# Kernel optimization log

Hardware: AMD Instinct MI355X
Metric: run time of the kernel (lower is better)

The kernel has to match this reference:

```python
import jax, jax.numpy as jnp
import numpy as np

D_MODEL = 256
NHEAD = 8
DHEAD = D_MODEL // NHEAD
LN_EPS = 1e-5
ATTN_EPS = 1e-6


def layer_norm(x, gamma, beta):
    mu = jnp.mean(x, axis=-1, keepdims=True)
    var = jnp.mean(jnp.square(x - mu), axis=-1, keepdims=True)
    return (x - mu) * jax.lax.rsqrt(var + LN_EPS) * gamma + beta


def setup_inputs() -> dict:
    key = jax.random.key(0)
    ks = jax.random.split(key, 12)
    B, L, S = 8, 4096, 4096
    s = 1.0 / np.sqrt(D_MODEL)
    return {
        "x": jax.random.normal(ks[0], (B, L, D_MODEL), jnp.float32),
        "source": jax.random.normal(ks[1], (B, S, D_MODEL), jnp.float32),
        "wq": jax.random.normal(ks[2], (D_MODEL, D_MODEL), jnp.float32) * s,
        "wk": jax.random.normal(ks[3], (D_MODEL, D_MODEL), jnp.float32) * s,
        "wv": jax.random.normal(ks[4], (D_MODEL, D_MODEL), jnp.float32) * s,
        "wmerge": jax.random.normal(ks[5], (D_MODEL, D_MODEL), jnp.float32) * s,
        "w1": jax.random.normal(ks[6], (2 * D_MODEL, D_MODEL), jnp.float32) * s,
        "w2": jax.random.normal(ks[7], (D_MODEL, 2 * D_MODEL), jnp.float32) * (1.0 / np.sqrt(2 * D_MODEL)),
        "g1": jnp.ones((D_MODEL,), jnp.float32),
        "b1": jnp.zeros((D_MODEL,), jnp.float32),
        "g2": jnp.ones((D_MODEL,), jnp.float32),
        "b2": jnp.zeros((D_MODEL,), jnp.float32),
    }


def reference(x, source, wq, wk, wv, wmerge, w1, w2, g1, b1, g2, b2):
    B, L, _ = x.shape
    S = source.shape[1]
    # QKV projections (bias-free Linear: y = x @ W^T), split into heads
    q = (x @ wq.T).reshape(B, L, NHEAD, DHEAD)
    k = (source @ wk.T).reshape(B, S, NHEAD, DHEAD)
    v = (source @ wv.T).reshape(B, S, NHEAD, DHEAD)
    # LinearAttention (LoFTR): feature map elu(.)+1, kernelized attention
    Q = jax.nn.elu(q) + 1.0
    K = jax.nn.elu(k) + 1.0
    v_len = jnp.asarray(S, v.dtype)
    values = v / v_len
    KV = jnp.einsum('bshd,bshv->bhdv', K, values)        # [B,H,D,D]
    Z = 1.0 / (jnp.einsum('blhd,bhd->blh', Q, K.sum(axis=1)) + ATTN_EPS)
    attended = jnp.einsum('blhd,bhdv,blh->blhv', Q, KV, Z) * v_len
    # merge + residual LN
    message = attended.reshape(B, L, D_MODEL) @ wmerge.T
    x = x + layer_norm(message, g1, b1)
    # MLP (d -> 2d -> d, ReLU) + residual LN
    h = jax.nn.relu(x @ w1.T) @ w2.T
    x = x + layer_norm(h, g2, b2)
    return x
```

## Files before the change

kernel.cpp:

```cpp
#include <hip/hip_runtime.h>

#define DM 256
#define SEQ 4096

typedef __attribute__((ext_vector_type(8))) short bf16x8;
typedef __attribute__((ext_vector_type(4))) float f32x4;

#define MFMA16(a, b, c) __builtin_amdgcn_mfma_f32_16x16x32_bf16(a, b, c, 0, 0, 0)

__device__ __forceinline__ short f2bf(float f) {
    union { float f; unsigned u; } c; c.f = f;
    unsigned r = (c.u + 0x7FFFu + ((c.u >> 16) & 1u)) >> 16;
    return (short)r;
}
__device__ __forceinline__ float bf2f(short s) {
    union { unsigned u; float f; } c; c.u = ((unsigned)(unsigned short)s) << 16; return c.f;
}
__device__ __forceinline__ bf16x8 pack8(float4 a, float4 b) {
    bf16x8 r;
    r[0] = f2bf(a.x); r[1] = f2bf(a.y); r[2] = f2bf(a.z); r[3] = f2bf(a.w);
    r[4] = f2bf(b.x); r[5] = f2bf(b.y); r[6] = f2bf(b.z); r[7] = f2bf(b.w);
    return r;
}

__global__ __launch_bounds__(256) void kWconv(const float* __restrict__ wq, const float* __restrict__ wk,
                                              const float* __restrict__ wv, const float* __restrict__ wm,
                                              const float* __restrict__ w1, const float* __restrict__ w2,
                                              short* __restrict__ dstws) {
    int blk = blockIdx.x;
    const float* src; short* dst;
    if (blk < 32)       { src = wq; dst = dstws;          }
    else if (blk < 64)  { src = wk; dst = dstws + 65536;  blk -= 32; }
    else if (blk < 96)  { src = wv; dst = dstws + 131072; blk -= 64; }
    else if (blk < 128) { src = wm; dst = dstws + 196608; blk -= 96; }
    else if (blk < 192) { src = w1; dst = dstws + 262144; blk -= 128; }
    else                { src = w2; dst = dstws + 393216; blk -= 192; }
    int idx = (blk * 256 + threadIdx.x) * 8;
    float4 f0 = *(const float4*)(src + idx), f1 = *(const float4*)(src + idx + 4);
    *(bf16x8*)(dst + idx) = pack8(f0, f1);
}

__global__ __launch_bounds__(256) void kA(const float* __restrict__ src,
                                          const short* __restrict__ wk, const short* __restrict__ wv,
                                          float* __restrict__ kv_part, float* __restrict__ ksum_part) {
    __shared__ char lds[65536];
    int t = threadIdx.x, lane = t & 63, w = t >> 6, r16 = lane & 15, g = lane >> 4;
    int b = blockIdx.x >> 6, blk = blockIdx.x & 63;
    const float* S = src + ((size_t)b * SEQ + blk * 64) * DM;
    char* kT = lds + w * 16384;
    char* vT = kT + 8192;
    f32x4 zz = {0.f, 0.f, 0.f, 0.f};
    f32x4 ak[4][4], av[4][4];
#pragma unroll
    for (int mi = 0; mi < 4; mi++)
#pragma unroll
        for (int ni = 0; ni < 4; ni++) { ak[mi][ni] = zz; av[mi][ni] = zz; }
#pragma unroll
    for (int kt = 0; kt < 8; kt++) {
        bf16x8 A[4], Bk[4], Bv[4];
#pragma unroll
        for (int mi = 0; mi < 4; mi++) {
            const float* p = S + (mi * 16 + r16) * DM + kt * 32 + g * 8;
            float4 f0 = *(const float4*)p, f1 = *(const float4*)(p + 4);
            A[mi] = pack8(f0, f1);
        }
#pragma unroll
        for (int ni = 0; ni < 4; ni++) {
            int n = w * 64 + ni * 16 + r16;
            Bk[ni] = *(const bf16x8*)(wk + n * DM + kt * 32 + g * 8);
            Bv[ni] = *(const bf16x8*)(wv + n * DM + kt * 32 + g * 8);
        }
#pragma unroll
        for (int mi = 0; mi < 4; mi++)
#pragma unroll
            for (int ni = 0; ni < 4; ni++) {
                ak[mi][ni] = MFMA16(A[mi], Bk[ni], ak[mi][ni]);
                av[mi][ni] = MFMA16(A[mi], Bv[ni], av[mi][ni]);
            }
    }
    float ksp[4] = {0.f, 0.f, 0.f, 0.f};
#pragma unroll
    for (int mi = 0; mi < 4; mi++)
#pragma unroll
        for (int ni = 0; ni < 4; ni++)
#pragma unroll
            for (int j = 0; j < 4; j++) {
                float q = ak[mi][ni][j];
                float e = q > 0.f ? q + 1.f : __expf(q);
                ksp[ni] += e;
                int srow = mi * 16 + g * 4 + j, feat = ni * 16 + r16;
                int by = (feat * 128 + srow * 2) ^ ((feat & 7) << 4);
                *(short*)(kT + by) = f2bf(e);
                *(short*)(vT + by) = f2bf(av[mi][ni][j]);
            }
    __syncthreads();
    f32x4 kv[2][2][2];
#pragma unroll
    for (int h = 0; h < 2; h++)
#pragma unroll
        for (int vi = 0; vi < 2; vi++)
#pragma unroll
            for (int di = 0; di < 2; di++) kv[h][vi][di] = zz;
#pragma unroll
    for (int h = 0; h < 2; h++)
#pragma unroll
        for (int st = 0; st < 2; st++) {
            bf16x8 Af[2], Bf[2];
#pragma unroll
            for (int vi = 0; vi < 2; vi++) {
                int row = h * 32 + vi * 16 + r16;
                Af[vi] = *(const bf16x8*)(vT + ((row * 128 + (st * 32 + g * 8) * 2) ^ ((row & 7) << 4)));
            }
#pragma unroll
            for (int di = 0; di < 2; di++) {
                int row = h * 32 + di * 16 + r16;
                Bf[di] = *(const bf16x8*)(kT + ((row * 128 + (st * 32 + g * 8) * 2) ^ ((row & 7) << 4)));
            }
#pragma unroll
            for (int vi = 0; vi < 2; vi++)
#pragma unroll
                for (int di = 0; di < 2; di++) kv[h][vi][di] = MFMA16(Af[vi], Bf[di], kv[h][vi][di]);
        }
    float* kvp = kv_part + ((size_t)(b * 64 + blk) * 8 + w * 2) * 1024;
#pragma unroll
    for (int h = 0; h < 2; h++)
#pragma unroll
        for (int vi = 0; vi < 2; vi++)
#pragma unroll
            for (int di = 0; di < 2; di++)
#pragma unroll
                for (int j = 0; j < 4; j++) {
                    int v = vi * 16 + g * 4 + j, d = di * 16 + r16;
                    kvp[h * 1024 + v * 32 + d] = kv[h][vi][di][j];
                }
#pragma unroll
    for (int ni = 0; ni < 4; ni++) {
        ksp[ni] += __shfl_xor(ksp[ni], 16);
        ksp[ni] += __shfl_xor(ksp[ni], 32);
    }
    if (lane < 16) {
        float* kp = ksum_part + (size_t)(b * 64 + blk) * 256 + w * 64;
#pragma unroll
        for (int ni = 0; ni < 4; ni++) kp[ni * 16 + lane] = ksp[ni];
    }
}

__global__ __launch_bounds__(256) void kA2(const float* __restrict__ kv_part, const float* __restrict__ ksum_part,
                                           short* __restrict__ kvt_bf, float* __restrict__ ksum) {
    int bh = blockIdx.x, b = bh >> 3, h = bh & 7, t = threadIdx.x;
#pragma unroll
    for (int i = 0; i < 4; i++) {
        int e = t + i * 256;
        float s = 0.f;
        for (int blk = 0; blk < 64; blk++)
            s += kv_part[((size_t)(b * 64 + blk) * 8 + h) * 1024 + e];
        kvt_bf[(size_t)bh * 1024 + e] = f2bf(s);
    }
    if (t < 32) {
        float s = 0.f;
        for (int blk = 0; blk < 64; blk++)
            s += ksum_part[(size_t)(b * 64 + blk) * 256 + h * 32 + t];
        ksum[bh * 32 + t] = s;
    }
}

__global__ __launch_bounds__(256) void kB(const float* __restrict__ x,
                                          const short* __restrict__ wq_bf, const short* __restrict__ wm_bf,
                                          const short* __restrict__ kvt_bf, const float* __restrict__ ksum,
                                          const float* __restrict__ g1, const float* __restrict__ b1,
                                          short* __restrict__ x1_ws) {
    __shared__ char xt[32768];
    __shared__ char qa[32768];
    __shared__ float ksum_l[256];
    __shared__ float red[64][4][2];
    int t = threadIdx.x, lane = t & 63, w = t >> 6, r16 = lane & 15, g = lane >> 4;
    int b = blockIdx.x >> 6, lb = blockIdx.x & 63, l0 = lb * 64;
    const float* xb = x + ((size_t)b * SEQ + l0) * DM;
    {
        int c8 = t & 31, r0 = t >> 5;
#pragma unroll
        for (int i = 0; i < 8; i++) {
            int row = r0 + i * 8;
            const float* p = xb + row * DM + c8 * 8;
            float4 f0 = *(const float4*)p, f1 = *(const float4*)(p + 4);
            int by = (row * 512 + c8 * 16) ^ ((row & 7) << 4);
            *(bf16x8*)(xt + by) = pack8(f0, f1);
        }
        ksum_l[t] = ksum[b * 256 + t];
    }
    __syncthreads();
    f32x4 zz = {0.f, 0.f, 0.f, 0.f};
    f32x4 acc[4][4];
#pragma unroll
    for (int mi = 0; mi < 4; mi++)
#pragma unroll
        for (int ni = 0; ni < 4; ni++) acc[mi][ni] = zz;
#pragma unroll
    for (int kt = 0; kt < 8; kt++) {
        bf16x8 A[4], Bf[4];
#pragma unroll
        for (int mi = 0; mi < 4; mi++) {
            int row = mi * 16 + r16;
            A[mi] = *(const bf16x8*)(xt + ((row * 512 + (kt * 32 + g * 8) * 2) ^ ((row & 7) << 4)));
        }
#pragma unroll
        for (int ni = 0; ni < 4; ni++)
            Bf[ni] = *(const bf16x8*)(wq_bf + (w * 64 + ni * 16 + r16) * DM + kt * 32 + g * 8);
#pragma unroll
        for (int mi = 0; mi < 4; mi++)
#pragma unroll
            for (int ni = 0; ni < 4; ni++) acc[mi][ni] = MFMA16(A[mi], Bf[ni], acc[mi][ni]);
    }
    float ks[2][2];
    ks[0][0] = ksum_l[(w * 2) * 32 + r16];     ks[0][1] = ksum_l[(w * 2) * 32 + 16 + r16];
    ks[1][0] = ksum_l[(w * 2 + 1) * 32 + r16]; ks[1][1] = ksum_l[(w * 2 + 1) * 32 + 16 + r16];
    float Zr[4][2][4];
#pragma unroll
    for (int mi = 0; mi < 4; mi++)
#pragma unroll
        for (int j = 0; j < 4; j++) {
#pragma unroll
            for (int ni = 0; ni < 4; ni++) {
                float q = acc[mi][ni][j];
                acc[mi][ni][j] = q > 0.f ? q + 1.f : __expf(q);
            }
            float d0 = acc[mi][0][j] * ks[0][0] + acc[mi][1][j] * ks[0][1];
            float d1 = acc[mi][2][j] * ks[1][0] + acc[mi][3][j] * ks[1][1];
#pragma unroll
            for (int m = 1; m < 16; m <<= 1) { d0 += __shfl_xor(d0, m); d1 += __shfl_xor(d1, m); }
            Zr[mi][0][j] = 1.f / (d0 + 1e-6f);
            Zr[mi][1][j] = 1.f / (d1 + 1e-6f);
        }
#pragma unroll
    for (int mi = 0; mi < 4; mi++)
#pragma unroll
        for (int ni = 0; ni < 4; ni++)
#pragma unroll
            for (int j = 0; j < 4; j++) {
                int row = mi * 16 + g * 4 + j, col = w * 64 + ni * 16 + r16;
                *(short*)(qa + ((row * 512 + col * 2) ^ ((row & 7) << 4))) = f2bf(acc[mi][ni][j]);
            }
    __syncthreads();
    f32x4 at[2][4][2];
#pragma unroll
    for (int h = 0; h < 2; h++)
#pragma unroll
        for (int mi = 0; mi < 4; mi++)
#pragma unroll
            for (int vi = 0; vi < 2; vi++) at[h][mi][vi] = zz;
#pragma unroll
    for (int h = 0; h < 2; h++) {
        int hh = w * 2 + h;
        bf16x8 A2[4], B2[2];
#pragma unroll
        for (int mi = 0; mi < 4; mi++) {
            int row = mi * 16 + r16, col = hh * 32 + g * 8;
            A2[mi] = *(const bf16x8*)(qa + ((row * 512 + col * 2) ^ ((row & 7) << 4)));
        }
        const short* kvb = kvt_bf + (size_t)(b * 8 + hh) * 1024;
#pragma unroll
        for (int vi = 0; vi < 2; vi++)
            B2[vi] = *(const bf16x8*)(kvb + (vi * 16 + r16) * 32 + g * 8);
#pragma unroll
        for (int mi = 0; mi < 4; mi++)
#pragma unroll
            for (int vi = 0; vi < 2; vi++) at[h][mi][vi] = MFMA16(A2[mi], B2[vi], at[h][mi][vi]);
    }
    __syncthreads();
#pragma unroll
    for (int h = 0; h < 2; h++)
#pragma unroll
        for (int mi = 0; mi < 4; mi++)
#pragma unroll
            for (int vi = 0; vi < 2; vi++)
#pragma unroll
                for (int j = 0; j < 4; j++) {
                    int row = mi * 16 + g * 4 + j, col = (w * 2 + h) * 32 + vi * 16 + r16;
                    float val = at[h][mi][vi][j] * Zr[mi][h][j];
                    *(short*)(qa + ((row * 512 + col * 2) ^ ((row & 7) << 4))) = f2bf(val);
                }
    __syncthreads();
    f32x4 am[4][4];
#pragma unroll
    for (int mi = 0; mi < 4; mi++)
#pragma unroll
        for (int ni = 0; ni < 4; ni++) am[mi][ni] = zz;
#pragma unroll
    for (int kt = 0; kt < 8; kt++) {
        bf16x8 A[4], Bf[4];
#pragma unroll
        for (int mi = 0; mi < 4; mi++) {
            int row = mi * 16 + r16;
            A[mi] = *(const bf16x8*)(qa + ((row * 512 + (kt * 32 + g * 8) * 2) ^ ((row & 7) << 4)));
        }
#pragma unroll
        for (int ni = 0; ni < 4; ni++)
            Bf[ni] = *(const bf16x8*)(wm_bf + (w * 64 + ni * 16 + r16) * DM + kt * 32 + g * 8);
#pragma unroll
        for (int mi = 0; mi < 4; mi++)
#pragma unroll
            for (int ni = 0; ni < 4; ni++) am[mi][ni] = MFMA16(A[mi], Bf[ni], am[mi][ni]);
    }
#pragma unroll
    for (int mi = 0; mi < 4; mi++)
#pragma unroll
        for (int j = 0; j < 4; j++) {
            float s = am[mi][0][j] + am[mi][1][j] + am[mi][2][j] + am[mi][3][j];
            float s2 = am[mi][0][j] * am[mi][0][j] + am[mi][1][j] * am[mi][1][j] +
                       am[mi][2][j] * am[mi][2][j] + am[mi][3][j] * am[mi][3][j];
#pragma unroll
            for (int m = 1; m < 16; m <<= 1) { s += __shfl_xor(s, m); s2 += __shfl_xor(s2, m); }
            if (r16 == 0) { int row = mi * 16 + g * 4 + j; red[row][w][0] = s; red[row][w][1] = s2; }
        }
    __syncthreads();
    float g1v[4], b1v[4];
#pragma unroll
    for (int ni = 0; ni < 4; ni++) { int col = w * 64 + ni * 16 + r16; g1v[ni] = g1[col]; b1v[ni] = b1[col]; }
#pragma unroll
    for (int mi = 0; mi < 4; mi++)
#pragma unroll
        for (int j = 0; j < 4; j++) {
            int row = mi * 16 + g * 4 + j;
            float mu = (red[row][0][0] + red[row][1][0] + red[row][2][0] + red[row][3][0]) * (1.f / DM);
            float ex2 = (red[row][0][1] + red[row][1][1] + red[row][2][1] + red[row][3][1]) * (1.f / DM);
            float rstd = rsqrtf(ex2 - mu * mu + 1e-5f);
#pragma unroll
            for (int ni = 0; ni < 4; ni++) {
                int col = w * 64 + ni * 16 + r16;
                float xv = bf2f(*(const short*)(xt + ((row * 512 + col * 2) ^ ((row & 7) << 4))));
                float x1v = xv + (am[mi][ni][j] - mu) * rstd * g1v[ni] + b1v[ni];
                *(short*)(qa + row * 512 + col * 2) = f2bf(x1v);
            }
        }
    __syncthreads();
    short* xop = x1_ws + ((size_t)b * SEQ + l0) * DM;
#pragma unroll
    for (int i = 0; i < 8; i++) {
        int idx = t + i * 256, row = idx >> 5, c8 = idx & 31;
        *(bf16x8*)(xop + row * DM + c8 * 8) = *(const bf16x8*)(qa + row * 512 + c8 * 16);
    }
}

__global__ __launch_bounds__(256) void kC(const short* __restrict__ x1_ws,
                                          const short* __restrict__ w1_bf, const short* __restrict__ w2_bf,
                                          const float* __restrict__ g2, const float* __restrict__ b2,
                                          float* __restrict__ out) {
    __shared__ char buf[65536];
    __shared__ float red[64][4][2];
    int t = threadIdx.x, lane = t & 63, w = t >> 6, r16 = lane & 15, g = lane >> 4;
    int b = blockIdx.x >> 6, lb = blockIdx.x & 63, l0 = lb * 64;
    const short* x1p = x1_ws + ((size_t)b * SEQ + l0) * DM;
#pragma unroll
    for (int i = 0; i < 8; i++) {
        int idx = t + i * 256, row = idx >> 5, c8 = idx & 31;
        bf16x8 v = *(const bf16x8*)(x1p + row * DM + c8 * 8);
        *(bf16x8*)(buf + ((row * 512 + c8 * 16) ^ ((row & 7) << 4))) = v;
    }
    __syncthreads();
    f32x4 zz = {0.f, 0.f, 0.f, 0.f};
    f32x4 a1[4][8];
#pragma unroll
    for (int mi = 0; mi < 4; mi++)
#pragma unroll
        for (int ni = 0; ni < 8; ni++) a1[mi][ni] = zz;
#pragma unroll
    for (int kt = 0; kt < 8; kt++) {
        bf16x8 A[4], Bf[8];
#pragma unroll
        for (int mi = 0; mi < 4; mi++) {
            int row = mi * 16 + r16;
            A[mi] = *(const bf16x8*)(buf + ((row * 512 + (kt * 32 + g * 8) * 2) ^ ((row & 7) << 4)));
        }
#pragma unroll
        for (int ni = 0; ni < 8; ni++)
            Bf[ni] = *(const bf16x8*)(w1_bf + (w * 128 + ni * 16 + r16) * DM + kt * 32 + g * 8);
#pragma unroll
        for (int mi = 0; mi < 4; mi++)
#pragma unroll
            for (int ni = 0; ni < 8; ni++) a1[mi][ni] = MFMA16(A[mi], Bf[ni], a1[mi][ni]);
    }
    __syncthreads();
#pragma unroll
    for (int mi = 0; mi < 4; mi++)
#pragma unroll
        for (int ni = 0; ni < 8; ni++)
#pragma unroll
            for (int j = 0; j < 4; j++) {
                float hv = a1[mi][ni][j]; hv = hv > 0.f ? hv : 0.f;
                int row = mi * 16 + g * 4 + j, col = w * 128 + ni * 16 + r16;
                *(short*)(buf + ((row * 1024 + col * 2) ^ ((row & 7) << 4))) = f2bf(hv);
            }
    __syncthreads();
    f32x4 a2[4][4];
#pragma unroll
    for (int mi = 0; mi < 4; mi++)
#pragma unroll
        for (int ni = 0; ni < 4; ni++) a2[mi][ni] = zz;
#pragma unroll
    for (int kt = 0; kt < 16; kt++) {
        bf16x8 A[4], Bf[4];
#pragma unroll
        for (int mi = 0; mi < 4; mi++) {
            int row = mi * 16 + r16;
            A[mi] = *(const bf16x8*)(buf + ((row * 1024 + (kt * 32 + g * 8) * 2) ^ ((row & 7) << 4)));
        }
#pragma unroll
        for (int ni = 0; ni < 4; ni++)
            Bf[ni] = *(const bf16x8*)(w2_bf + (w * 64 + ni * 16 + r16) * 512 + kt * 32 + g * 8);
#pragma unroll
        for (int mi = 0; mi < 4; mi++)
#pragma unroll
            for (int ni = 0; ni < 4; ni++) a2[mi][ni] = MFMA16(A[mi], Bf[ni], a2[mi][ni]);
    }
#pragma unroll
    for (int mi = 0; mi < 4; mi++)
#pragma unroll
        for (int j = 0; j < 4; j++) {
            float s = a2[mi][0][j] + a2[mi][1][j] + a2[mi][2][j] + a2[mi][3][j];
            float s2 = a2[mi][0][j] * a2[mi][0][j] + a2[mi][1][j] * a2[mi][1][j] +
                       a2[mi][2][j] * a2[mi][2][j] + a2[mi][3][j] * a2[mi][3][j];
#pragma unroll
            for (int m = 1; m < 16; m <<= 1) { s += __shfl_xor(s, m); s2 += __shfl_xor(s2, m); }
            if (r16 == 0) { int row = mi * 16 + g * 4 + j; red[row][w][0] = s; red[row][w][1] = s2; }
        }
    __syncthreads();
    float g2v[4], b2v[4];
#pragma unroll
    for (int ni = 0; ni < 4; ni++) { int col = w * 64 + ni * 16 + r16; g2v[ni] = g2[col]; b2v[ni] = b2[col]; }
#pragma unroll
    for (int mi = 0; mi < 4; mi++)
#pragma unroll
        for (int j = 0; j < 4; j++) {
            int row = mi * 16 + g * 4 + j;
            float mu = (red[row][0][0] + red[row][1][0] + red[row][2][0] + red[row][3][0]) * (1.f / DM);
            float ex2 = (red[row][0][1] + red[row][1][1] + red[row][2][1] + red[row][3][1]) * (1.f / DM);
            float rstd = rsqrtf(ex2 - mu * mu + 1e-5f);
#pragma unroll
            for (int ni = 0; ni < 4; ni++) {
                int col = w * 64 + ni * 16 + r16;
                float ln = (a2[mi][ni][j] - mu) * rstd * g2v[ni] + b2v[ni];
                *(float*)(buf + row * 1024 + col * 4) = ln;
            }
        }
    __syncthreads();
    float* op = out + ((size_t)b * SEQ + l0) * DM;
#pragma unroll
    for (int i = 0; i < 16; i++) {
        int idx = t + i * 256, row = idx >> 6, c4 = idx & 63;
        float4 f = *(const float4*)(buf + row * 1024 + c4 * 16);
        short4 xs = *(const short4*)(x1p + row * DM + c4 * 4);
        f.x += bf2f(xs.x); f.y += bf2f(xs.y); f.z += bf2f(xs.z); f.w += bf2f(xs.w);
        *(float4*)(op + row * DM + c4 * 4) = f;
    }
}

extern "C" void kernel_launch(void* const* d_in, const int* in_sizes, int n_in,
                              void* d_out, int out_size, void* d_ws, size_t ws_size,
                              hipStream_t stream) {
    const float* x   = (const float*)d_in[0];
    const float* src = (const float*)d_in[1];
    const float* wq  = (const float*)d_in[2];
    const float* wk  = (const float*)d_in[3];
    const float* wv  = (const float*)d_in[4];
    const float* wm  = (const float*)d_in[5];
    const float* w1  = (const float*)d_in[6];
    const float* w2  = (const float*)d_in[7];
    const float* g1  = (const float*)d_in[8];
    const float* b1  = (const float*)d_in[9];
    const float* g2  = (const float*)d_in[10];
    const float* b2  = (const float*)d_in[11];
    float* out = (float*)d_out;

    char* ws = (char*)d_ws;
    short* w_bf      = (short*)ws;
    short* kvt_bf    = (short*)(ws + 1048576);
    float* ksum      = (float*)(ws + 1179648);
    short* x1_ws     = (short*)(ws + 1187840);
    float* kv_part   = (float*)(ws + 17965056);
    float* ksum_part = (float*)(ws + 34742272);

    kWconv<<<256, 256, 0, stream>>>(wq, wk, wv, wm, w1, w2, w_bf);
    kA<<<512, 256, 0, stream>>>(src, w_bf + 65536, w_bf + 131072, kv_part, ksum_part);
    kA2<<<64, 256, 0, stream>>>(kv_part, ksum_part, kvt_bf, ksum);
    kB<<<512, 256, 0, stream>>>(x, w_bf, w_bf + 196608, kvt_bf, ksum, g1, b1, x1_ws);
    kC<<<512, 256, 0, stream>>>(x1_ws, w_bf + 262144, w_bf + 393216, g2, b2, out);
}
```

Measured before the change: 264.8 us.

## Fuse attention-output and MLP kernels, stage source tile in LDS, widen blocks

Merges the query/attention/merge+LN1 kernel and the MLP+LN2 kernel into one kernel that works on 32-row tiles with 512 threads. This removes the bf16 x1 round trip through global memory and one launch. The K/V projection kernel now stages the source tile once in swizzled LDS as bf16 and uses 8 waves, each owning one head. The KV reduction kernel is split across 4x more blocks with unrolled partial sums. In exchange, weight operands are reloaded from global per smaller tile, and the larger blocks raise register and LDS pressure.

Result: faster. 247.7 us (-6.5%).

```diff
diff --git a/kernel.cpp b/kernel.cpp
--- a/kernel.cpp
+++ b/kernel.cpp
@@ -40,49 +40,56 @@
     *(bf16x8*)(dst + idx) = pack8(f0, f1);
 }
 
-__global__ __launch_bounds__(256) void kA(const float* __restrict__ src,
-                                          const short* __restrict__ wk, const short* __restrict__ wv,
-                                          float* __restrict__ kv_part, float* __restrict__ ksum_part) {
+__global__ __launch_bounds__(512, 4) void kA(const float* __restrict__ src,
+                                             const short* __restrict__ wk, const short* __restrict__ wv,
+                                             float* __restrict__ kv_part, float* __restrict__ ksum_part) {
     __shared__ char lds[65536];
     int t = threadIdx.x, lane = t & 63, w = t >> 6, r16 = lane & 15, g = lane >> 4;
     int b = blockIdx.x >> 6, blk = blockIdx.x & 63;
     const float* S = src + ((size_t)b * SEQ + blk * 64) * DM;
-    char* kT = lds + w * 16384;
-    char* vT = kT + 8192;
+#pragma unroll
+    for (int i = 0; i < 4; i++) {
+        int chunk = t + i * 512, row = chunk >> 5, c8 = chunk & 31;
+        const float* p = S + row * DM + c8 * 8;
+        float4 f0 = *(const float4*)p, f1 = *(const float4*)(p + 4);
+        int by = (row * 512 + c8 * 16) ^ ((row & 7) << 4);
+        *(bf16x8*)(lds + by) = pack8(f0, f1);
+    }
+    __syncthreads();
     f32x4 zz = {0.f, 0.f, 0.f, 0.f};
-    f32x4 ak[4][4], av[4][4];
+    f32x4 ak[4][2], av[4][2];
 #pragma unroll
     for (int mi = 0; mi < 4; mi++)
 #pragma unroll
-        for (int ni = 0; ni < 4; ni++) { ak[mi][ni] = zz; av[mi][ni] = zz; }
+        for (int ni = 0; ni < 2; ni++) { ak[mi][ni] = zz; av[mi][ni] = zz; }
 #pragma unroll
     for (int kt = 0; kt < 8; kt++) {
-        bf16x8 A[4], Bk[4], Bv[4];
+        bf16x8 A[4];
 #pragma unroll
         for (int mi = 0; mi < 4; mi++) {
-            const float* p = S + (mi * 16 + r16) * DM + kt * 32 + g * 8;
-            float4 f0 = *(const float4*)p, f1 = *(const float4*)(p + 4);
-            A[mi] = pack8(f0, f1);
-        }
-#pragma unroll
-        for (int ni = 0; ni < 4; ni++) {
-            int n = w * 64 + ni * 16 + r16;
-            Bk[ni] = *(const bf16x8*)(wk + n * DM + kt * 32 + g * 8);
-            Bv[ni] = *(const bf16x8*)(wv + n * DM + kt * 32 + g * 8);
-        }
-#pragma unroll
-        for (int mi = 0; mi < 4; mi++)
-#pragma unroll
-            for (int ni = 0; ni < 4; ni++) {
-                ak[mi][ni] = MFMA16(A[mi], Bk[ni], ak[mi][ni]);
-                av[mi][ni] = MFMA16(A[mi], Bv[ni], av[mi][ni]);
-            }
-    }
-    float ksp[4] = {0.f, 0.f, 0.f, 0.f};
+            int row = mi * 16 + r16;
+            A[mi] = *(const bf16x8*)(lds + ((row * 512 + (kt * 32 + g * 8) * 2) ^ ((row & 7) << 4)));
+        }
+#pragma unroll
+        for (int ni = 0; ni < 2; ni++) {
+            int n = w * 32 + ni * 16 + r16;
+            bf16x8 Bk = *(const bf16x8*)(wk + n * DM + kt * 32 + g * 8);
+            bf16x8 Bv = *(const bf16x8*)(wv + n * DM + kt * 32 + g * 8);
+#pragma unroll
+            for (int mi = 0; mi < 4; mi++) {
+                ak[mi][ni] = MFMA16(A[mi], Bk, ak[mi][ni]);
+                av[mi][ni] = MFMA16(A[mi], Bv, av[mi][ni]);
+            }
+        }
+    }
+    __syncthreads();
+    char* kT = lds + w * 8192;
+    char* vT = kT + 4096;
+    float ksp[2] = {0.f, 0.f};
 #pragma unroll
     for (int mi = 0; mi < 4; mi++)
 #pragma unroll
-        for (int ni = 0; ni < 4; ni++)
+        for (int ni = 0; ni < 2; ni++)
 #pragma unroll
             for (int j = 0; j < 4; j++) {
                 float q = ak[mi][ni][j];
@@ -94,363 +101,314 @@
                 *(short*)(vT + by) = f2bf(av[mi][ni][j]);
             }
     __syncthreads();
-    f32x4 kv[2][2][2];
-#pragma unroll
-    for (int h = 0; h < 2; h++)
+    f32x4 kv[2][2];
+#pragma unroll
+    for (int vi = 0; vi < 2; vi++)
+#pragma unroll
+        for (int di = 0; di < 2; di++) kv[vi][di] = zz;
+#pragma unroll
+    for (int st = 0; st < 2; st++) {
+        bf16x8 Af[2], Bf[2];
+#pragma unroll
+        for (int vi = 0; vi < 2; vi++) {
+            int row = vi * 16 + r16;
+            Af[vi] = *(const bf16x8*)(vT + ((row * 128 + (st * 32 + g * 8) * 2) ^ ((row & 7) << 4)));
+            Bf[vi] = *(const bf16x8*)(kT + ((row * 128 + (st * 32 + g * 8) * 2) ^ ((row & 7) << 4)));
+        }
 #pragma unroll
         for (int vi = 0; vi < 2; vi++)
 #pragma unroll
-            for (int di = 0; di < 2; di++) kv[h][vi][di] = zz;
-#pragma unroll
-    for (int h = 0; h < 2; h++)
-#pragma unroll
-        for (int st = 0; st < 2; st++) {
-            bf16x8 Af[2], Bf[2];
-#pragma unroll
-            for (int vi = 0; vi < 2; vi++) {
-                int row = h * 32 + vi * 16 + r16;
-                Af[vi] = *(const bf16x8*)(vT + ((row * 128 + (st * 32 + g * 8) * 2) ^ ((row & 7) << 4)));
-            }
-#pragma unroll
-            for (int di = 0; di < 2; di++) {
-                int row = h * 32 + di * 16 + r16;
-                Bf[di] = *(const bf16x8*)(kT + ((row * 128 + (st * 32 + g * 8) * 2) ^ ((row & 7) << 4)));
-            }
-#pragma unroll
-            for (int vi = 0; vi < 2; vi++)
-#pragma unroll
-                for (int di = 0; di < 2; di++) kv[h][vi][di] = MFMA16(Af[vi], Bf[di], kv[h][vi][di]);
-        }
-    float* kvp = kv_part + ((size_t)(b * 64 + blk) * 8 + w * 2) * 1024;
-#pragma unroll
-    for (int h = 0; h < 2; h++)
-#pragma unroll
-        for (int vi = 0; vi < 2; vi++)
-#pragma unroll
-            for (int di = 0; di < 2; di++)
-#pragma unroll
-                for (int j = 0; j < 4; j++) {
-                    int v = vi * 16 + g * 4 + j, d = di * 16 + r16;
-                    kvp[h * 1024 + v * 32 + d] = kv[h][vi][di][j];
-                }
-#pragma unroll
-    for (int ni = 0; ni < 4; ni++) {
+            for (int di = 0; di < 2; di++) kv[vi][di] = MFMA16(Af[vi], Bf[di], kv[vi][di]);
+    }
+    float* kvp = kv_part + ((size_t)(b * 64 + blk) * 8 + w) * 1024;
+#pragma unroll
+    for (int vi = 0; vi < 2; vi++)
+#pragma unroll
+        for (int di = 0; di < 2; di++)
+#pragma unroll
+            for (int j = 0; j < 4; j++) {
+                int v = vi * 16 + g * 4 + j, d = di * 16 + r16;
+                kvp[v * 32 + d] = kv[vi][di][j];
+            }
+#pragma unroll
+    for (int ni = 0; ni < 2; ni++) {
         ksp[ni] += __shfl_xor(ksp[ni], 16);
         ksp[ni] += __shfl_xor(ksp[ni], 32);
     }
     if (lane < 16) {
-        float* kp = ksum_part + (size_t)(b * 64 + blk) * 256 + w * 64;
-#pragma unroll
-        for (int ni = 0; ni < 4; ni++) kp[ni * 16 + lane] = ksp[ni];
+        float* kp = ksum_part + (size_t)(b * 64 + blk) * 256 + w * 32;
+#pragma unroll
+        for (int ni = 0; ni < 2; ni++) kp[ni * 16 + lane] = ksp[ni];
     }
 }
 
 __global__ __launch_bounds__(256) void kA2(const float* __restrict__ kv_part, const float* __restrict__ ksum_part,
                                            short* __restrict__ kvt_bf, float* __restrict__ ksum) {
-    int bh = blockIdx.x, b = bh >> 3, h = bh & 7, t = threadIdx.x;
-#pragma unroll
-    for (int i = 0; i < 4; i++) {
-        int e = t + i * 256;
+    int blk = blockIdx.x, t = threadIdx.x;
+    int b = blk >> 5, h = (blk >> 2) & 7, q = blk & 3;
+    int e = q * 256 + t;
+    float s0 = 0.f, s1 = 0.f, s2 = 0.f, s3 = 0.f;
+    for (int bk = 0; bk < 64; bk += 4) {
+        s0 += kv_part[((size_t)(b * 64 + bk) * 8 + h) * 1024 + e];
+        s1 += kv_part[((size_t)(b * 64 + bk + 1) * 8 + h) * 1024 + e];
+        s2 += kv_part[((size_t)(b * 64 + bk + 2) * 8 + h) * 1024 + e];
+        s3 += kv_part[((size_t)(b * 64 + bk + 3) * 8 + h) * 1024 + e];
+    }
+    kvt_bf[(size_t)(b * 8 + h) * 1024 + e] = f2bf((s0 + s1) + (s2 + s3));
+    if (q == 3 && t < 32) {
         float s = 0.f;
-        for (int blk = 0; blk < 64; blk++)
-            s += kv_part[((size_t)(b * 64 + blk) * 8 + h) * 1024 + e];
-        kvt_bf[(size_t)bh * 1024 + e] = f2bf(s);
-    }
-    if (t < 32) {
-        float s = 0.f;
-        for (int blk = 0; blk < 64; blk++)
-            s += ksum_part[(size_t)(b * 64 + blk) * 256 + h * 32 + t];
-        ksum[bh * 32 + t] = s;
-    }
-}
-
-__global__ __launch_bounds__(256) void kB(const float* __restrict__ x,
-                                          const short* __restrict__ wq_bf, const short* __restrict__ wm_bf,
-                                          const short* __restrict__ kvt_bf, const float* __restrict__ ksum,
-                                          const float* __restrict__ g1, const float* __restrict__ b1,
-                                          short* __restrict__ x1_ws) {
-    __shared__ char xt[32768];
-    __shared__ char qa[32768];
-    __shared__ float ksum_l[256];
-    __shared__ float red[64][4][2];
+        for (int bk = 0; bk < 64; bk++)
+            s += ksum_part[(size_t)(b * 64 + bk) * 256 + h * 32 + t];
+        ksum[(b * 8 + h) * 32 + t] = s;
+    }
+}
+
+__global__ __launch_bounds__(512, 4) void kBC(const float* __restrict__ x,
+                                              const short* __restrict__ wq_bf, const short* __restrict__ wm_bf,
+                                              const short* __restrict__ w1_bf, const short* __restrict__ w2_bf,
+                                              const short* __restrict__ kvt_bf, const float* __restrict__ ksum,
+                                              const float* __restrict__ g1, const float* __restrict__ b1,
+                                              const float* __restrict__ g2, const float* __restrict__ b2,
+                                              float* __restrict__ out) {
+    __shared__ char lds[52224];
+    char* xt = lds;
+    char* hb = lds + 16384;
+    char* qa = lds + 16384;
+    float* red = (float*)(lds + 49152);
+    float* ksl = (float*)(lds + 51200);
     int t = threadIdx.x, lane = t & 63, w = t >> 6, r16 = lane & 15, g = lane >> 4;
-    int b = blockIdx.x >> 6, lb = blockIdx.x & 63, l0 = lb * 64;
+    int b = blockIdx.x >> 7, lb = blockIdx.x & 127, l0 = lb * 32;
     const float* xb = x + ((size_t)b * SEQ + l0) * DM;
-    {
-        int c8 = t & 31, r0 = t >> 5;
-#pragma unroll
-        for (int i = 0; i < 8; i++) {
-            int row = r0 + i * 8;
-            const float* p = xb + row * DM + c8 * 8;
-            float4 f0 = *(const float4*)p, f1 = *(const float4*)(p + 4);
-            int by = (row * 512 + c8 * 16) ^ ((row & 7) << 4);
-            *(bf16x8*)(xt + by) = pack8(f0, f1);
-        }
-        ksum_l[t] = ksum[b * 256 + t];
-    }
+#pragma unroll
+    for (int i = 0; i < 2; i++) {
+        int chunk = t + i * 512, row = chunk >> 5, c8 = chunk & 31;
+        const float* p = xb + row * DM + c8 * 8;
+        float4 f0 = *(const float4*)p, f1 = *(const float4*)(p + 4);
+        int by = (row * 512 + c8 * 16) ^ ((row & 7) << 4);
+        *(bf16x8*)(xt + by) = pack8(f0, f1);
+    }
+    if (t < 256) ksl[t] = ksum[b * 256 + t];
     __syncthreads();
     f32x4 zz = {0.f, 0.f, 0.f, 0.f};
-    f32x4 acc[4][4];
-#pragma unroll
-    for (int mi = 0; mi < 4; mi++)
-#pragma unroll
-        for (int ni = 0; ni < 4; ni++) acc[mi][ni] = zz;
+    f32x4 acc[2][2];
+#pragma unroll
+    for (int mi = 0; mi < 2; mi++)
+#pragma unroll
+        for (int ni = 0; ni < 2; ni++) acc[mi][ni] = zz;
 #pragma unroll
     for (int kt = 0; kt < 8; kt++) {
-        bf16x8 A[4], Bf[4];
-#pragma unroll
-        for (int mi = 0; mi < 4; mi++) {
+        bf16x8 A[2], Bf[2];
+#pragma unroll
+        for (int mi = 0; mi < 2; mi++) {
             int row = mi * 16 + r16;
             A[mi] = *(const bf16x8*)(xt + ((row * 512 + (kt * 32 + g * 8) * 2) ^ ((row & 7) << 4)));
         }
 #pragma unroll
-        for (int ni = 0; ni < 4; ni++)
-            Bf[ni] = *(const bf16x8*)(wq_bf + (w * 64 + ni * 16 + r16) * DM + kt * 32 + g * 8);
-#pragma unroll
-        for (int mi = 0; mi < 4; mi++)
-#pragma unroll
-            for (int ni = 0; ni < 4; ni++) acc[mi][ni] = MFMA16(A[mi], Bf[ni], acc[mi][ni]);
-    }
-    float ks[2][2];
-    ks[0][0] = ksum_l[(w * 2) * 32 + r16];     ks[0][1] = ksum_l[(w * 2) * 32 + 16 + r16];
-    ks[1][0] = ksum_l[(w * 2 + 1) * 32 + r16]; ks[1][1] = ksum_l[(w * 2 + 1) * 32 + 16 + r16];
-    float Zr[4][2][4];
-#pragma unroll
-    for (int mi = 0; mi < 4; mi++)
+        for (int ni = 0; ni < 2; ni++)
+            Bf[ni] = *(const bf16x8*)(wq_bf + (w * 32 + ni * 16 + r16) * DM + kt * 32 + g * 8);
+#pragma unroll
+        for (int mi = 0; mi < 2; mi++)
+#pragma unroll
+            for (int ni = 0; ni < 2; ni++) acc[mi][ni] = MFMA16(A[mi], Bf[ni], acc[mi][ni]);
+    }
+    float ks0 = ksl[w * 32 + r16], ks1 = ksl[w * 32 + 16 + r16];
+    float Zr[2][4];
+#pragma unroll
+    for (int mi = 0; mi < 2; mi++)
 #pragma unroll
         for (int j = 0; j < 4; j++) {
 #pragma unroll
-            for (int ni = 0; ni < 4; ni++) {
+            for (int ni = 0; ni < 2; ni++) {
                 float q = acc[mi][ni][j];
                 acc[mi][ni][j] = q > 0.f ? q + 1.f : __expf(q);
             }
-            float d0 = acc[mi][0][j] * ks[0][0] + acc[mi][1][j] * ks[0][1];
-            float d1 = acc[mi][2][j] * ks[1][0] + acc[mi][3][j] * ks[1][1];
-#pragma unroll
-            for (int m = 1; m < 16; m <<= 1) { d0 += __shfl_xor(d0, m); d1 += __shfl_xor(d1, m); }
-            Zr[mi][0][j] = 1.f / (d0 + 1e-6f);
-            Zr[mi][1][j] = 1.f / (d1 + 1e-6f);
-        }
-#pragma unroll
-    for (int mi = 0; mi < 4; mi++)
-#pragma unroll
-        for (int ni = 0; ni < 4; ni++)
-#pragma unroll
-            for (int j = 0; j < 4; j++) {
-                int row = mi * 16 + g * 4 + j, col = w * 64 + ni * 16 + r16;
+            float d0 = acc[mi][0][j] * ks0 + acc[mi][1][j] * ks1;
+#pragma unroll
+            for (int m = 1; m < 16; m <<= 1) d0 += __shfl_xor(d0, m);
+            Zr[mi][j] = 1.f / (d0 + 1e-6f);
+        }
+#pragma unroll
+    for (int mi = 0; mi < 2; mi++)
+#pragma unroll
+        for (int ni = 0; ni < 2; ni++)
+#pragma unroll
+            for (int j = 0; j < 4; j++) {
+                int row = mi * 16 + g * 4 + j, col = w * 32 + ni * 16 + r16;
                 *(short*)(qa + ((row * 512 + col * 2) ^ ((row & 7) << 4))) = f2bf(acc[mi][ni][j]);
             }
-    __syncthreads();
-    f32x4 at[2][4][2];
-#pragma unroll
-    for (int h = 0; h < 2; h++)
-#pragma unroll
-        for (int mi = 0; mi < 4; mi++)
-#pragma unroll
-            for (int vi = 0; vi < 2; vi++) at[h][mi][vi] = zz;
-#pragma unroll
-    for (int h = 0; h < 2; h++) {
-        int hh = w * 2 + h;
-        bf16x8 A2[4], B2[2];
-#pragma unroll
-        for (int mi = 0; mi < 4; mi++) {
-            int row = mi * 16 + r16, col = hh * 32 + g * 8;
+    f32x4 at[2][2];
+#pragma unroll
+    for (int mi = 0; mi < 2; mi++)
+#pragma unroll
+        for (int vi = 0; vi < 2; vi++) at[mi][vi] = zz;
+    {
+        bf16x8 A2[2], B2[2];
+#pragma unroll
+        for (int mi = 0; mi < 2; mi++) {
+            int row = mi * 16 + r16, col = w * 32 + g * 8;
             A2[mi] = *(const bf16x8*)(qa + ((row * 512 + col * 2) ^ ((row & 7) << 4)));
         }
-        const short* kvb = kvt_bf + (size_t)(b * 8 + hh) * 1024;
+        const short* kvb = kvt_bf + (size_t)(b * 8 + w) * 1024;
 #pragma unroll
         for (int vi = 0; vi < 2; vi++)
             B2[vi] = *(const bf16x8*)(kvb + (vi * 16 + r16) * 32 + g * 8);
 #pragma unroll
-        for (int mi = 0; mi < 4; mi++)
-#pragma unroll
-            for (int vi = 0; vi < 2; vi++) at[h][mi][vi] = MFMA16(A2[mi], B2[vi], at[h][mi][vi]);
-    }
-    __syncthreads();
-#pragma unroll
-    for (int h = 0; h < 2; h++)
-#pragma unroll
-        for (int mi = 0; mi < 4; mi++)
-#pragma unroll
-            for (int vi = 0; vi < 2; vi++)
-#pragma unroll
-                for (int j = 0; j < 4; j++) {
-                    int row = mi * 16 + g * 4 + j, col = (w * 2 + h) * 32 + vi * 16 + r16;
-                    float val = at[h][mi][vi][j] * Zr[mi][h][j];
-                    *(short*)(qa + ((row * 512 + col * 2) ^ ((row & 7) << 4))) = f2bf(val);
-                }
-    __syncthreads();
-    f32x4 am[4][4];
-#pragma unroll
-    for (int mi = 0; mi < 4; mi++)
-#pragma unroll
-        for (int ni = 0; ni < 4; ni++) am[mi][ni] = zz;
+        for (int mi = 0; mi < 2; mi++)
+#pragma unroll
+            for (int vi = 0; vi < 2; vi++) at[mi][vi] = MFMA16(A2[mi], B2[vi], at[mi][vi]);
+    }
+#pragma unroll
+    for (int mi = 0; mi < 2; mi++)
+#pragma unroll
+        for (int vi = 0; vi < 2; vi++)
+#pragma unroll
+            for (int j = 0; j < 4; j++) {
+                int row = mi * 16 + g * 4 + j, col = w * 32 + vi * 16 + r16;
+                *(short*)(qa + ((row * 512 + col * 2) ^ ((row & 7) << 4))) = f2bf(at[mi][vi][j] * Zr[mi][j]);
+            }
+    __syncthreads();
+    f32x4 am[2][2];
+#pragma unroll
+    for (int mi = 0; mi < 2; mi++)
+#pragma unroll
+        for (int ni = 0; ni < 2; ni++) am[mi][ni] = zz;
 #pragma unroll
     for (int kt = 0; kt < 8; kt++) {
-        bf16x8 A[4], Bf[4];
-#pragma unroll
-        for (int mi = 0; mi < 4; mi++) {
+        bf16x8 A[2], Bf[2];
+#pragma unroll
+        for (int mi = 0; mi < 2; mi++) {
             int row = mi * 16 + r16;
             A[mi] = *(const bf16x8*)(qa + ((row * 512 + (kt * 32 + g * 8) * 2) ^ ((row & 7) << 4)));
         }
 #pragma unroll
+        for (int ni = 0; ni < 2; ni++)
+            Bf[ni] = *(const bf16x8*)(wm_bf + (w * 32 + ni * 16 + r16) * DM + kt * 32 + g * 8);
+#pragma unroll
+        for (int mi = 0; mi < 2; mi++)
+#pragma unroll
+            for (int ni = 0; ni < 2; ni++) am[mi][ni] = MFMA16(A[mi], Bf[ni], am[mi][ni]);
+    }
+#pragma unroll
+    for (int mi = 0; mi < 2; mi++)
+#pragma unroll
+        for (int j = 0; j < 4; j++) {
+            float s = am[mi][0][j] + am[mi][1][j];
+            float s2 = am[mi][0][j] * am[mi][0][j] + am[mi][1][j] * am[mi][1][j];
+#pragma unroll
+            for (int m = 1; m < 16; m <<= 1) { s += __shfl_xor(s, m); s2 += __shfl_xor(s2, m); }
+            if (r16 == 0) { int row = mi * 16 + g * 4 + j; red[(row * 8 + w) * 2] = s; red[(row * 8 + w) * 2 + 1] = s2; }
+        }
+    __syncthreads();
+    {
+        float g1v[2], b1v[2];
+#pragma unroll
+        for (int ni = 0; ni < 2; ni++) { int col = w * 32 + ni * 16 + r16; g1v[ni] = g1[col]; b1v[ni] = b1[col]; }
+#pragma unroll
+        for (int mi = 0; mi < 2; mi++)
+#pragma unroll
+            for (int j = 0; j < 4; j++) {
+                int row = mi * 16 + g * 4 + j;
+                float mu = 0.f, ex2 = 0.f;
+#pragma unroll
+                for (int ww = 0; ww < 8; ww++) { mu += red[(row * 8 + ww) * 2]; ex2 += red[(row * 8 + ww) * 2 + 1]; }
+                mu *= (1.f / DM); ex2 *= (1.f / DM);
+                float rstd = rsqrtf(ex2 - mu * mu + 1e-5f);
+#pragma unroll
+                for (int ni = 0; ni < 2; ni++) {
+                    int col = w * 32 + ni * 16 + r16;
+                    int by = (row * 512 + col * 2) ^ ((row & 7) << 4);
+                    float xv = bf2f(*(const short*)(xt + by));
+                    *(short*)(xt + by) = f2bf(xv + (am[mi][ni][j] - mu) * rstd * g1v[ni] + b1v[ni]);
+                }
+            }
+    }
+    __syncthreads();
+    f32x4 a1[2][4];
+#pragma unroll
+    for (int mi = 0; mi < 2; mi++)
+#pragma unroll
+        for (int ni = 0; ni < 4; ni++) a1[mi][ni] = zz;
+#pragma unroll
+    for (int kt = 0; kt < 8; kt++) {
+        bf16x8 A[2], Bf[4];
+#pragma unroll
+        for (int mi = 0; mi < 2; mi++) {
+            int row = mi * 16 + r16;
+            A[mi] = *(const bf16x8*)(xt + ((row * 512 + (kt * 32 + g * 8) * 2) ^ ((row & 7) << 4)));
+        }
+#pragma unroll
         for (int ni = 0; ni < 4; ni++)
-            Bf[ni] = *(const bf16x8*)(wm_bf + (w * 64 + ni * 16 + r16) * DM + kt * 32 + g * 8);
-#pragma unroll
-        for (int mi = 0; mi < 4; mi++)
-#pragma unroll
-            for (int ni = 0; ni < 4; ni++) am[mi][ni] = MFMA16(A[mi], Bf[ni], am[mi][ni]);
-    }
-#pragma unroll
-    for (int mi = 0; mi < 4; mi++)
+            Bf[ni] = *(const bf16x8*)(w1_bf + (w * 64 + ni * 16 + r16) * DM + kt * 32 + g * 8);
+#pragma unroll
+        for (int mi = 0; mi < 2; mi++)
+#pragma unroll
+            for (int ni = 0; ni < 4; ni++) a1[mi][ni] = MFMA16(A[mi], Bf[ni], a1[mi][ni]);
+    }
+#pragma unroll
+    for (int mi = 0; mi < 2; mi++)
+#pragma unroll
+        for (int ni = 0; ni < 4; ni++)
+#pragma unroll
+            for (int j = 0; j < 4; j++) {
+                float hv = a1[mi][ni][j]; hv = hv > 0.f ? hv : 0.f;
+                int row = mi * 16 + g * 4 + j, col = w * 64 + ni * 16 + r16;
+                *(short*)(hb + ((row * 1024 + col * 2) ^ ((row & 7) << 4))) = f2bf(hv);
+            }
+    __syncthreads();
+    f32x4 a2[2][2];
+#pragma unroll
+    for (int mi = 0; mi < 2; mi++)
+#pragma unroll
+        for (int ni = 0; ni < 2; ni++) a2[mi][ni] = zz;
+#pragma unroll
+    for (int kt = 0; kt < 16; kt++) {
+        bf16x8 A[2], Bf[2];
+#pragma unroll
+        for (int mi = 0; mi < 2; mi++) {
+            int row = mi * 16 + r16;
+            A[mi] = *(const bf16x8*)(hb + ((row * 1024 + (kt * 32 + g * 8) * 2) ^ ((row & 7) << 4)));
+        }
+#pragma unroll
+        for (int ni = 0; ni < 2; ni++)
+            Bf[ni] = *(const bf16x8*)(w2_bf + (w * 32 + ni * 16 + r16) * 512 + kt * 32 + g * 8);
+#pragma unroll
+        for (int mi = 0; mi < 2; mi++)
+#pragma unroll
+            for (int ni = 0; ni < 2; ni++) a2[mi][ni] = MFMA16(A[mi], Bf[ni], a2[mi][ni]);
+    }
+#pragma unroll
+    for (int mi = 0; mi < 2; mi++)
 #pragma unroll
         for (int j = 0; j < 4; j++) {
-            float s = am[mi][0][j] + am[mi][1][j] + am[mi][2][j] + am[mi][3][j];
-            float s2 = am[mi][0][j] * am[mi][0][j] + am[mi][1][j] * am[mi][1][j] +
-                       am[mi][2][j] * am[mi][2][j] + am[mi][3][j] * am[mi][3][j];
+            float s = a2[mi][0][j] + a2[mi][1][j];
+            float s2 = a2[mi][0][j] * a2[mi][0][j] + a2[mi][1][j] * a2[mi][1][j];
 #pragma unroll
             for (int m = 1; m < 16; m <<= 1) { s += __shfl_xor(s, m); s2 += __shfl_xor(s2, m); }
-            if (r16 == 0) { int row = mi * 16 + g * 4 + j; red[row][w][0] = s; red[row][w][1] = s2; }
-        }
-    __syncthreads();
-    float g1v[4], b1v[4];
-#pragma unroll
-    for (int ni = 0; ni < 4; ni++) { int col = w * 64 + ni * 16 + r16; g1v[ni] = g1[col]; b1v[ni] = b1[col]; }
-#pragma unroll
-    for (int mi = 0; mi < 4; mi++)
-#pragma unroll
-        for (int j = 0; j < 4; j++) {
-            int row = mi * 16 + g * 4 + j;
-            float mu = (red[row][0][0] + red[row][1][0] + red[row][2][0] + red[row][3][0]) * (1.f / DM);
-            float ex2 = (red[row][0][1] + red[row][1][1] + red[row][2][1] + red[row][3][1]) * (1.f / DM);
-            float rstd = rsqrtf(ex2 - mu * mu + 1e-5f);
-#pragma unroll
-            for (int ni = 0; ni < 4; ni++) {
-                int col = w * 64 + ni * 16 + r16;
-                float xv = bf2f(*(const short*)(xt + ((row * 512 + col * 2) ^ ((row & 7) << 4))));
-                float x1v = xv + (am[mi][ni][j] - mu) * rstd * g1v[ni] + b1v[ni];
-                *(short*)(qa + row * 512 + col * 2) = f2bf(x1v);
-            }
-        }
-    __syncthreads();
-    short* xop = x1_ws + ((size_t)b * SEQ + l0) * DM;
-#pragma unroll
-    for (int i = 0; i < 8; i++) {
-        int idx = t + i * 256, row = idx >> 5, c8 = idx & 31;
-        *(bf16x8*)(xop + row * DM + c8 * 8) = *(const bf16x8*)(qa + row * 512 + c8 * 16);
-    }
-}
-
-__global__ __launch_bounds__(256) void kC(const short* __restrict__ x1_ws,
-                                          const short* __restrict__ w1_bf, const short* __restrict__ w2_bf,
-                                          const float* __restrict__ g2, const float* __restrict__ b2,
-                                          float* __restrict__ out) {
-    __shared__ char buf[65536];
-    __shared__ float red[64][4][2];
-    int t = threadIdx.x, lane = t & 63, w = t >> 6, r16 = lane & 15, g = lane >> 4;
-    int b = blockIdx.x >> 6, lb = blockIdx.x & 63, l0 = lb * 64;
-    const short* x1p = x1_ws + ((size_t)b * SEQ + l0) * DM;
-#pragma unroll
-    for (int i = 0; i < 8; i++) {
-        int idx = t + i * 256, row = idx >> 5, c8 = idx & 31;
-        bf16x8 v = *(const bf16x8*)(x1p + row * DM + c8 * 8);
-        *(bf16x8*)(buf + ((row * 512 + c8 * 16) ^ ((row & 7) << 4))) = v;
-    }
-    __syncthreads();
-    f32x4 zz = {0.f, 0.f, 0.f, 0.f};
-    f32x4 a1[4][8];
-#pragma unroll
-    for (int mi = 0; mi < 4; mi++)
-#pragma unroll
-        for (int ni = 0; ni < 8; ni++) a1[mi][ni] = zz;
-#pragma unroll
-    for (int kt = 0; kt < 8; kt++) {
-        bf16x8 A[4], Bf[8];
-#pragma unroll
-        for (int mi = 0; mi < 4; mi++) {
-            int row = mi * 16 + r16;
-            A[mi] = *(const bf16x8*)(buf + ((row * 512 + (kt * 32 + g * 8) * 2) ^ ((row & 7) << 4)));
-        }
-#pragma unroll
-        for (int ni = 0; ni < 8; ni++)
-            Bf[ni] = *(const bf16x8*)(w1_bf + (w * 128 + ni * 16 + r16) * DM + kt * 32 + g * 8);
-#pragma unroll
-        for (int mi = 0; mi < 4; mi++)
-#pragma unroll
-            for (int ni = 0; ni < 8; ni++) a1[mi][ni] = MFMA16(A[mi], Bf[ni], a1[mi][ni]);
-    }
-    __syncthreads();
-#pragma unroll
-    for (int mi = 0; mi < 4; mi++)
-#pragma unroll
-        for (int ni = 0; ni < 8; ni++)
-#pragma unroll
-            for (int j = 0; j < 4; j++) {
-                float hv = a1[mi][ni][j]; hv = hv > 0.f ? hv : 0.f;
-                int row = mi * 16 + g * 4 + j, col = w * 128 + ni * 16 + r16;
-                *(short*)(buf + ((row * 1024 + col * 2) ^ ((row & 7) << 4))) = f2bf(hv);
-            }
-    __syncthreads();
-    f32x4 a2[4][4];
-#pragma unroll
-    for (int mi = 0; mi < 4; mi++)
-#pragma unroll
-        for (int ni = 0; ni < 4; ni++) a2[mi][ni] = zz;
-#pragma unroll
-    for (int kt = 0; kt < 16; kt++) {
-        bf16x8 A[4], Bf[4];
-#pragma unroll
-        for (int mi = 0; mi < 4; mi++) {
-            int row = mi * 16 + r16;
-            A[mi] = *(const bf16x8*)(buf + ((row * 1024 + (kt * 32 + g * 8) * 2) ^ ((row & 7) << 4)));
-        }
-#pragma unroll
-        for (int ni = 0; ni < 4; ni++)
-            Bf[ni] = *(const bf16x8*)(w2_bf + (w * 64 + ni * 16 + r16) * 512 + kt * 32 + g * 8);
-#pragma unroll
-        for (int mi = 0; mi < 4; mi++)
-#pragma unroll
-            for (int ni = 0; ni < 4; ni++) a2[mi][ni] = MFMA16(A[mi], Bf[ni], a2[mi][ni]);
-    }
-#pragma unroll
-    for (int mi = 0; mi < 4; mi++)
-#pragma unroll
-        for (int j = 0; j < 4; j++) {
-            float s = a2[mi][0][j] + a2[mi][1][j] + a2[mi][2][j] + a2[mi][3][j];
-            float s2 = a2[mi][0][j] * a2[mi][0][j] + a2[mi][1][j] * a2[mi][1][j] +
-                       a2[mi][2][j] * a2[mi][2][j] + a2[mi][3][j] * a2[mi][3][j];
-#pragma unroll
-            for (int m = 1; m < 16; m <<= 1) { s += __shfl_xor(s, m); s2 += __shfl_xor(s2, m); }
-            if (r16 == 0) { int row = mi * 16 + g * 4 + j; red[row][w][0] = s; red[row][w][1] = s2; }
-        }
-    __syncthreads();
-    float g2v[4], b2v[4];
-#pragma unroll
-    for (int ni = 0; ni < 4; ni++) { int col = w * 64 + ni * 16 + r16; g2v[ni] = g2[col]; b2v[ni] = b2[col]; }
-#pragma unroll
-    for (int mi = 0; mi < 4; mi++)
-#pragma unroll
-        for (int j = 0; j < 4; j++) {
-            int row = mi * 16 + g * 4 + j;
-            float mu = (red[row][0][0] + red[row][1][0] + red[row][2][0] + red[row][3][0]) * (1.f / DM);
-            float ex2 = (red[row][0][1] + red[row][1][1] + red[row][2][1] + red[row][3][1]) * (1.f / DM);
-            float rstd = rsqrtf(ex2 - mu * mu + 1e-5f);
-#pragma unroll
-            for (int ni = 0; ni < 4; ni++) {
-                int col = w * 64 + ni * 16 + r16;
-                float ln = (a2[mi][ni][j] - mu) * rstd * g2v[ni] + b2v[ni];
-                *(float*)(buf + row * 1024 + col * 4) = ln;
-            }
-        }
-    __syncthreads();
-    float* op = out + ((size_t)b * SEQ + l0) * DM;
-#pragma unroll
-    for (int i = 0; i < 16; i++) {
-        int idx = t + i * 256, row = idx >> 6, c4 = idx & 63;
-        float4 f = *(const float4*)(buf + row * 1024 + c4 * 16);
-        short4 xs = *(const short4*)(x1p + row * DM + c4 * 4);
-        f.x += bf2f(xs.x); f.y += bf2f(xs.y); f.z += bf2f(xs.z); f.w += bf2f(xs.w);
-        *(float4*)(op + row * DM + c4 * 4) = f;
+            if (r16 == 0) { int row = mi * 16 + g * 4 + j; red[(row * 8 + w) * 2] = s; red[(row * 8 + w) * 2 + 1] = s2; }
+        }
+    __syncthreads();
+    {
+        float g2v[2], b2v[2];
+#pragma unroll
+        for (int ni = 0; ni < 2; ni++) { int col = w * 32 + ni * 16 + r16; g2v[ni] = g2[col]; b2v[ni] = b2[col]; }
+        float* op = out + ((size_t)b * SEQ + l0) * DM;
+#pragma unroll
+        for (int mi = 0; mi < 2; mi++)
+#pragma unroll
+            for (int j = 0; j < 4; j++) {
+                int row = mi * 16 + g * 4 + j;
+                float mu = 0.f, ex2 = 0.f;
+#pragma unroll
+                for (int ww = 0; ww < 8; ww++) { mu += red[(row * 8 + ww) * 2]; ex2 += red[(row * 8 + ww) * 2 + 1]; }
+                mu *= (1.f / DM); ex2 *= (1.f / DM);
+                float rstd = rsqrtf(ex2 - mu * mu + 1e-5f);
+#pragma unroll
+                for (int ni = 0; ni < 2; ni++) {
+                    int col = w * 32 + ni * 16 + r16;
+                    float xv = bf2f(*(const short*)(xt + ((row * 512 + col * 2) ^ ((row & 7) << 4))));
+                    op[row * DM + col] = xv + (a2[mi][ni][j] - mu) * rstd * g2v[ni] + b2v[ni];
+                }
+            }
     }
 }
 
@@ -475,13 +433,12 @@
     short* w_bf      = (short*)ws;
     short* kvt_bf    = (short*)(ws + 1048576);
     float* ksum      = (float*)(ws + 1179648);
-    short* x1_ws     = (short*)(ws + 1187840);
-    float* kv_part   = (float*)(ws + 17965056);
-    float* ksum_part = (float*)(ws + 34742272);
+    float* kv_part   = (float*)(ws + 1187840);
+    float* ksum_part = (float*)(ws + 17965056);
 
     kWconv<<<256, 256, 0, stream>>>(wq, wk, wv, wm, w1, w2, w_bf);
-    kA<<<512, 256, 0, stream>>>(src, w_bf + 65536, w_bf + 131072, kv_part, ksum_part);
-    kA2<<<64, 256, 0, stream>>>(kv_part, ksum_part, kvt_bf, ksum);
-    kB<<<512, 256, 0, stream>>>(x, w_bf, w_bf + 196608, kvt_bf, ksum, g1, b1, x1_ws);
-    kC<<<512, 256, 0, stream>>>(x1_ws, w_bf + 262144, w_bf + 393216, g2, b2, out);
-}
+    kA<<<512, 512, 0, stream>>>(src, w_bf + 65536, w_bf + 131072, kv_part, ksum_part);
+    kA2<<<256, 256, 0, stream>>>(kv_part, ksum_part, kvt_bf, ksum);
+    kBC<<<1024, 512, 0, stream>>>(x, w_bf, w_bf + 196608, w_bf + 262144, w_bf + 393216,
+                                  kvt_bf, ksum, g1, b1, g2, b2, out);
+}
```
